# Kernel optimization log

Measured on AMD Instinct MI355X. Metric: run time of the kernel, lower is better.

The kernel has to match this reference:

```python
import jax, jax.numpy as jnp
import numpy as np

HIDDEN = 2048
HEADS = 16
HEAD_DIM = HIDDEN // HEADS
BATCH = 2
SEQ = 2048
ROPE_BASE = 10000.0


def _rope_cos_sin(seq_len, head_dim, dtype):
    inv_freq = 1.0 / (ROPE_BASE ** (jnp.arange(0, head_dim, 2, dtype=jnp.float32) / head_dim))
    t = jnp.arange(seq_len, dtype=jnp.float32)
    freqs = jnp.outer(t, inv_freq)                 # [S, D/2]
    emb = jnp.concatenate([freqs, freqs], axis=-1)  # [S, D]
    return jnp.cos(emb).astype(dtype), jnp.sin(emb).astype(dtype)


def _rotate_half(x):
    x1, x2 = jnp.split(x, 2, axis=-1)
    return jnp.concatenate([-x2, x1], axis=-1)


def setup_inputs() -> dict:
    key = jax.random.key(0)
    ks = jax.random.split(key, 5)
    scale = 1.0 / np.sqrt(HIDDEN)
    return {
        "x": jax.random.normal(ks[0], (BATCH, SEQ, HIDDEN), dtype=jnp.float32),
        "Wq": jax.random.normal(ks[1], (HIDDEN, HIDDEN), dtype=jnp.float32) * scale,
        "Wk": jax.random.normal(ks[2], (HIDDEN, HIDDEN), dtype=jnp.float32) * scale,
        "Wv": jax.random.normal(ks[3], (HIDDEN, HIDDEN), dtype=jnp.float32) * scale,
        "Wo": jax.random.normal(ks[4], (HIDDEN, HIDDEN), dtype=jnp.float32) * scale,
    }


def reference(x, Wq, Wk, Wv, Wo):
    B, S, H = x.shape
    # projections (torch Linear: y = x @ W.T)
    q = jnp.einsum('bsh,oh->bso', x, Wq).reshape(B, S, HEADS, HEAD_DIM).transpose(0, 2, 1, 3)
    k = jnp.einsum('bsh,oh->bso', x, Wk).reshape(B, S, HEADS, HEAD_DIM).transpose(0, 2, 1, 3)
    v = jnp.einsum('bsh,oh->bso', x, Wv).reshape(B, S, HEADS, HEAD_DIM).transpose(0, 2, 1, 3)
    # RoPE
    cos, sin = _rope_cos_sin(S, HEAD_DIM, x.dtype)  # [S, D]
    cos = cos[None, None]  # [1,1,S,D]
    sin = sin[None, None]
    q = q * cos + _rotate_half(q) * sin
    k = k * cos + _rotate_half(k) * sin
    # attention scores [B, H, S, S]
    scale = HEAD_DIM ** -0.5
    scores = jnp.einsum('bhqd,bhkd->bhqk', q, k) * scale
    causal = jnp.triu(jnp.ones((S, S), dtype=bool), k=1)  # kv_len==seq -> diagonal=1
    scores = jnp.where(causal[None, None], -jnp.inf, scores)
    attn = jax.nn.softmax(scores.astype(jnp.float32), axis=-1).astype(q.dtype)
    # dropout is identity in eval mode
    out = jnp.einsum('bhqk,bhkd->bhqd', attn, v)  # [B,H,S,D]
    out = out.transpose(0, 2, 1, 3).reshape(B, S, H)
    return jnp.einsum('bsh,oh->bso', out, Wo)
```

## Files before the change

kernel.cpp:

```cpp
#include <hip/hip_runtime.h>
#include <hip/hip_bf16.h>
#include <cstdint>
#include <cstddef>

constexpr int HIDDEN = 2048;
constexpr int HEADS  = 16;
constexpr int HD     = 128;
constexpr int BATCH  = 2;
constexpr int SEQ    = 2048;
constexpr int MROWS  = BATCH * SEQ;

typedef __attribute__((ext_vector_type(8))) short bf16x8;
typedef __attribute__((ext_vector_type(4))) float f32x4;

__device__ __forceinline__ unsigned short f2bf(float f) {
  union { float f; unsigned int u; } c; c.f = f;
  unsigned int r = c.u + 0x7FFFu + ((c.u >> 16) & 1u);
  return (unsigned short)(r >> 16);
}
__device__ __forceinline__ unsigned short f2bft(float f) {
  union { float f; unsigned int u; } c; c.f = f;
  return (unsigned short)(c.u >> 16);
}
__device__ __forceinline__ float bf2f(unsigned short u) {
  union { unsigned int u; float f; } c; c.u = ((unsigned int)u) << 16;
  return c.f;
}

__device__ __forceinline__ void gload_lds16(const void* g, void* l) {
  __builtin_amdgcn_global_load_lds(
      (const __attribute__((address_space(1))) void*)g,
      (__attribute__((address_space(3))) void*)l, 16, 0, 0);
}

__global__ void k_cvt(const float* __restrict__ in, unsigned short* __restrict__ out, int n4) {
  int i = blockIdx.x * 256 + threadIdx.x;
  if (i >= n4) return;
  float4 v = reinterpret_cast<const float4*>(in)[i];
  ushort4 o;
  o.x = f2bf(v.x); o.y = f2bf(v.y); o.z = f2bf(v.z); o.w = f2bf(v.w);
  reinterpret_cast<ushort4*>(out)[i] = o;
}

__global__ void k_cvtw(const float* __restrict__ w0, const float* __restrict__ w1,
                       const float* __restrict__ w2, const float* __restrict__ w3,
                       unsigned short* __restrict__ out) {
  constexpr int N4W = HIDDEN * HIDDEN / 4;
  int idx = blockIdx.x * 256 + threadIdx.x;
  int seg = idx >> 20;
  int off = idx & (N4W - 1);
  const float* src = (seg == 0) ? w0 : (seg == 1) ? w1 : (seg == 2) ? w2 : w3;
  float4 v = reinterpret_cast<const float4*>(src)[off];
  ushort4 o;
  o.x = f2bf(v.x); o.y = f2bf(v.y); o.z = f2bf(v.z); o.w = f2bf(v.w);
  reinterpret_cast<ushort4*>(out)[idx] = o;
}

template<int MODE>
__global__ __launch_bounds__(256, 2) void k_gemm(const unsigned short* __restrict__ A,
                                                 const unsigned short* __restrict__ Bm,
                                                 void* __restrict__ Cout,
                                                 int M, int N, int K) {
  __shared__ unsigned short As[128 * 32];
  __shared__ unsigned short Bs[128 * 32];
  const int t    = threadIdx.x;
  const int lane = t & 63;
  const int w    = t >> 6;
  const int wr   = w >> 1, wc = w & 1;
  const int m0   = blockIdx.y * 128;
  const int n0   = blockIdx.x * 128;
  const int l15  = lane & 15, lg = lane >> 4;

  f32x4 acc[4][4];
#pragma unroll
  for (int mi = 0; mi < 4; ++mi)
#pragma unroll
    for (int ni = 0; ni < 4; ++ni)
#pragma unroll
      for (int r = 0; r < 4; ++r) acc[mi][ni][r] = 0.f;

  const int rowA = t >> 2;
  const int col8 = (t & 3) * 8;
  const unsigned short* gA0 = A  + (size_t)(m0 + rowA) * K + col8;
  const unsigned short* gA1 = gA0 + (size_t)64 * K;
  const unsigned short* gB0 = Bm + (size_t)(n0 + rowA) * K + col8;
  const unsigned short* gB1 = gB0 + (size_t)64 * K;
  unsigned short* lA0 = As + t * 8;
  unsigned short* lA1 = As + 64 * 32 + t * 8;
  unsigned short* lB0 = Bs + t * 8;
  unsigned short* lB1 = Bs + 64 * 32 + t * 8;

  for (int k0 = 0; k0 < K; k0 += 32) {
    gload_lds16(gA0 + k0, lA0);
    gload_lds16(gA1 + k0, lA1);
    gload_lds16(gB0 + k0, lB0);
    gload_lds16(gB1 + k0, lB1);
    __syncthreads();

    bf16x8 a[4], b[4];
#pragma unroll
    for (int i = 0; i < 4; ++i)
      a[i] = *reinterpret_cast<const bf16x8*>(&As[(wr * 64 + i * 16 + l15) * 32 + lg * 8]);
#pragma unroll
    for (int i = 0; i < 4; ++i)
      b[i] = *reinterpret_cast<const bf16x8*>(&Bs[(wc * 64 + i * 16 + l15) * 32 + lg * 8]);
#pragma unroll
    for (int mi = 0; mi < 4; ++mi)
#pragma unroll
      for (int ni = 0; ni < 4; ++ni)
        acc[mi][ni] = __builtin_amdgcn_mfma_f32_16x16x32_bf16(a[mi], b[ni], acc[mi][ni], 0, 0, 0);
    __syncthreads();
  }

#pragma unroll
  for (int mi = 0; mi < 4; ++mi) {
#pragma unroll
    for (int ni = 0; ni < 4; ++ni) {
#pragma unroll
      for (int r = 0; r < 4; ++r) {
        int row = m0 + wr * 64 + mi * 16 + lg * 4 + r;
        int col = n0 + wc * 64 + ni * 16 + l15;
        float v = acc[mi][ni][r];
        if (MODE == 2) {
          reinterpret_cast<float*>(Cout)[(size_t)row * N + col] = v;
        } else if (MODE == 0) {
          int b = row >> 11, s = row & (SEQ - 1);
          int which = col >> 11;
          int hc = col & 2047;
          int h = hc >> 7, d = hc & (HD - 1);
          size_t addr = (size_t)which * ((size_t)MROWS * HIDDEN)
                      + ((size_t)(b * HEADS + h) * SEQ + s) * HD + d;
          reinterpret_cast<unsigned short*>(Cout)[addr] = f2bf(v);
        } else {
          int h = row >> 7, d = row & (HD - 1);
          int b = col >> 11, s = col & (SEQ - 1);
          size_t addr = ((size_t)(b * HEADS + h) * HD + d) * SEQ + s;
          reinterpret_cast<unsigned short*>(Cout)[addr] = f2bf(v);
        }
      }
    }
  }
}

constexpr float QSCALE = 0.08838834764831845f * 1.4426950408889634f;

__global__ void k_rope(unsigned short* __restrict__ Qb, unsigned short* __restrict__ Kb) {
  int idx = blockIdx.x * 256 + threadIdx.x;
  int c  = idx & 7;
  int s  = (idx >> 3) & (SEQ - 1);
  int bh = idx >> 14;
  size_t base = ((size_t)bh * SEQ + s) * HD + c * 8;

  bf16x8 ql = *reinterpret_cast<const bf16x8*>(Qb + base);
  bf16x8 qh = *reinterpret_cast<const bf16x8*>(Qb + base + 64);
  bf16x8 kl = *reinterpret_cast<const bf16x8*>(Kb + base);
  bf16x8 kh = *reinterpret_cast<const bf16x8*>(Kb + base + 64);
  bf16x8 qlo, qho, klo, kho;
#pragma unroll
  for (int j = 0; j < 8; ++j) {
    float d   = (float)(c * 8 + j);
    float ang = (float)s * expf(d * -0.14391156511756683f);
    float sn, cs;
    __sincosf(ang, &sn, &cs);
    float a0 = bf2f((unsigned short)ql[j]), a1 = bf2f((unsigned short)qh[j]);
    qlo[j] = (short)f2bf((a0 * cs - a1 * sn) * QSCALE);
    qho[j] = (short)f2bf((a1 * cs + a0 * sn) * QSCALE);
    float b0 = bf2f((unsigned short)kl[j]), b1 = bf2f((unsigned short)kh[j]);
    klo[j] = (short)f2bf(b0 * cs - b1 * sn);
    kho[j] = (short)f2bf(b1 * cs + b0 * sn);
  }
  *reinterpret_cast<bf16x8*>(Qb + base)      = qlo;
  *reinterpret_cast<bf16x8*>(Qb + base + 64) = qho;
  *reinterpret_cast<bf16x8*>(Kb + base)      = klo;
  *reinterpret_cast<bf16x8*>(Kb + base + 64) = kho;
}

constexpr int QB  = 128;
constexpr int KVB = 64;
constexpr int NQT = SEQ / QB;

__global__ __launch_bounds__(512)
__attribute__((amdgpu_waves_per_eu(4, 4)))
void k_attn(const unsigned short* __restrict__ Q,
            const unsigned short* __restrict__ Kk,
            const unsigned short* __restrict__ Vt,
            unsigned short* __restrict__ O) {
  __shared__ char lds[2 * 16384 + 2 * 16384 + 16384];
  char* Ks = lds;
  char* Vs = lds + 2 * 16384;
  char* Ps = lds + 4 * 16384;

  const int t    = threadIdx.x;
  const int lane = t & 63;
  const int w    = t >> 6;
  const int l15  = lane & 15, lg = lane >> 4;
  const int bh   = blockIdx.y;
  const int b    = bh >> 4, h = bh & 15;
  const int qt   = (bh >= HEADS) ? (NQT - 1 - (int)blockIdx.x) : (int)blockIdx.x;
  const int q0b  = qt * QB;
  const int q0w  = q0b + w * 16;
  const int qw_hi = q0w + 15;

  const unsigned short* Qb = Q  + (size_t)bh * SEQ * HD;
  const unsigned short* Kb = Kk + (size_t)bh * SEQ * HD;
  const unsigned short* Vb = Vt + (size_t)bh * HD * SEQ;

  bf16x8 qf[4];
#pragma unroll
  for (int c = 0; c < 4; ++c)
    qf[c] = *reinterpret_cast<const bf16x8*>(Qb + (size_t)(q0w + l15) * HD + c * 32 + lg * 8);

  float mrow[4], lpart[4];
  f32x4 oacc[8];
#pragma unroll
  for (int r = 0; r < 4; ++r) { mrow[r] = -1e30f; lpart[r] = 0.f; }
#pragma unroll
  for (int dt = 0; dt < 8; ++dt)
#pragma unroll
    for (int r = 0; r < 4; ++r) oacc[dt][r] = 0.f;

  const int sp     = t * 16;
  const int srow   = sp >> 8;
  const int scolb  = (sp & 255) ^ ((srow & 7) << 4);
  const unsigned short* ksrc2 = Kb + (size_t)srow * HD + (scolb >> 1);
  char* kdst2 = Ks + sp;

  const int vrow  = t >> 3;
  const int vcolb = ((t & 7) << 4) ^ ((vrow & 7) << 4);
  const unsigned short* vsrc = Vb + (size_t)vrow * SEQ + (vcolb >> 1);
  char* vdst = Vs + t * 16;

  const int nb = q0b / KVB + 2;

  gload_lds16(ksrc2, kdst2);
  gload_lds16(ksrc2 + (size_t)32 * HD, kdst2 + 8192);
  gload_lds16(vsrc, vdst);
  gload_lds16(vsrc + (size_t)64 * SEQ, vdst + 8192);
  __syncthreads();

  int cur = 0;
  for (int kb = 0; kb < nb; ++kb) {
    const int kv0 = kb * KVB;
    if (kb + 1 < nb) {
      const int nxt = kv0 + KVB;
      char* nk = kdst2 + (cur ^ 1) * 16384;
      char* nv = vdst  + (cur ^ 1) * 16384;
      gload_lds16(ksrc2 + (size_t)nxt * HD, nk);
      gload_lds16(ksrc2 + (size_t)(nxt + 32) * HD, nk + 8192);
      gload_lds16(vsrc + nxt, nv);
      gload_lds16(vsrc + (size_t)64 * SEQ + nxt, nv + 8192);
    }

    if (kv0 <= qw_hi) {
      const char* Kc = Ks + cur * 16384;
      const char* Vc = Vs + cur * 16384;
      f32x4 sc[4];
#pragma unroll
      for (int tt = 0; tt < 4; ++tt)
#pragma unroll
        for (int r = 0; r < 4; ++r) sc[tt][r] = 0.f;
      __builtin_amdgcn_s_setprio(1);
#pragma unroll
      for (int tt = 0; tt < 4; ++tt) {
        const int kr = tt * 16 + l15;
        const int xr = (kr & 7) << 4;
#pragma unroll
        for (int c = 0; c < 4; ++c) {
          bf16x8 kf = *reinterpret_cast<const bf16x8*>(
              Kc + kr * 256 + ((c * 64 + lg * 16) ^ xr));
          sc[tt] = __builtin_amdgcn_mfma_f32_16x16x32_bf16(qf[c], kf, sc[tt], 0, 0, 0);
        }
      }
      __builtin_amdgcn_s_setprio(0);

      const bool full = (kv0 + KVB - 1 <= q0w);
#pragma unroll
      for (int r = 0; r < 4; ++r) {
        const int qg = q0w + lg * 4 + r;
        float v0 = sc[0][r], v1 = sc[1][r];
        float v2 = sc[2][r], v3 = sc[3][r];
        if (!full) {
          if (kv0 +      l15 > qg) v0 = -1e30f;
          if (kv0 + 16 + l15 > qg) v1 = -1e30f;
          if (kv0 + 32 + l15 > qg) v2 = -1e30f;
          if (kv0 + 48 + l15 > qg) v3 = -1e30f;
        }
        float pm = fmaxf(fmaxf(v0, v1), fmaxf(v2, v3));
        if (__any(pm > mrow[r] + 11.5f)) {
          float pmr = pm;
          pmr = fmaxf(pmr, __shfl_xor(pmr, 1));
          pmr = fmaxf(pmr, __shfl_xor(pmr, 2));
          pmr = fmaxf(pmr, __shfl_xor(pmr, 4));
          pmr = fmaxf(pmr, __shfl_xor(pmr, 8));
          float mn = fmaxf(mrow[r], pmr);
          float al = exp2f(mrow[r] - mn);
          lpart[r] *= al;
#pragma unroll
          for (int dt = 0; dt < 8; ++dt) oacc[dt][r] *= al;
          mrow[r] = mn;
        }
        float p0 = exp2f(v0 - mrow[r]);
        float p1 = exp2f(v1 - mrow[r]);
        float p2 = exp2f(v2 - mrow[r]);
        float p3 = exp2f(v3 - mrow[r]);
        lpart[r] += (p0 + p1) + (p2 + p3);
        const int prow = lg * 4 + r;
        const int xpr  = (prow & 7) << 4;
        char* pw = Ps + w * 2048 + prow * 128;
        *reinterpret_cast<unsigned short*>(pw + (((0 * 32) + l15 * 2) ^ xpr)) = f2bft(p0);
        *reinterpret_cast<unsigned short*>(pw + (((1 * 32) + l15 * 2) ^ xpr)) = f2bft(p1);
        *reinterpret_cast<unsigned short*>(pw + (((2 * 32) + l15 * 2) ^ xpr)) = f2bft(p2);
        *reinterpret_cast<unsigned short*>(pw + (((3 * 32) + l15 * 2) ^ xpr)) = f2bft(p3);
      }
      asm volatile("s_waitcnt lgkmcnt(0)" ::: "memory");

      const int xq = (l15 & 7) << 4;
      const char* pr = Ps + w * 2048 + l15 * 128;
      bf16x8 pa0 = *reinterpret_cast<const bf16x8*>(pr + ((0  + lg * 16) ^ xq));
      bf16x8 pa1 = *reinterpret_cast<const bf16x8*>(pr + ((64 + lg * 16) ^ xq));
      const int xv = (l15 & 7) << 4;
      __builtin_amdgcn_s_setprio(1);
#pragma unroll
      for (int dt = 0; dt < 8; ++dt) {
        const char* vrl = Vc + (dt * 16 + l15) * 128;
        bf16x8 vf0 = *reinterpret_cast<const bf16x8*>(vrl + ((lg * 16) ^ xv));
        bf16x8 vf1 = *reinterpret_cast<const bf16x8*>(vrl + ((64 + lg * 16) ^ xv));
        oacc[dt] = __builtin_amdgcn_mfma_f32_16x16x32_bf16(pa0, vf0, oacc[dt], 0, 0, 0);
        oacc[dt] = __builtin_amdgcn_mfma_f32_16x16x32_bf16(pa1, vf1, oacc[dt], 0, 0, 0);
      }
      __builtin_amdgcn_s_setprio(0);
    }
    __syncthreads();
    cur ^= 1;
  }

  float inv[4];
#pragma unroll
  for (int r = 0; r < 4; ++r) {
    float ls = lpart[r];
    ls += __shfl_xor(ls, 1);
    ls += __shfl_xor(ls, 2);
    ls += __shfl_xor(ls, 4);
    ls += __shfl_xor(ls, 8);
    inv[r] = 1.0f / ls;
  }
#pragma unroll
  for (int dt = 0; dt < 8; ++dt) {
#pragma unroll
    for (int r = 0; r < 4; ++r) {
      int qg = q0w + lg * 4 + r;
      int dv = dt * 16 + l15;
      O[((size_t)(b * SEQ + qg) * HEADS + h) * HD + dv] = f2bf(oacc[dt][r] * inv[r]);
    }
  }
}

extern "C" void kernel_launch(void* const* d_in, const int* in_sizes, int n_in,
                              void* d_out, int out_size, void* d_ws, size_t ws_size,
                              hipStream_t stream) {
  (void)in_sizes; (void)n_in; (void)out_size; (void)ws_size;
  const float* x  = (const float*)d_in[0];
  const float* Wq = (const float*)d_in[1];
  const float* Wk = (const float*)d_in[2];
  const float* Wv = (const float*)d_in[3];
  const float* Wo = (const float*)d_in[4];
  float* out = (float*)d_out;

  unsigned short* xb  = (unsigned short*)d_ws;
  unsigned short* wqb = xb  + (size_t)MROWS * HIDDEN;
  unsigned short* wkb = wqb + (size_t)HIDDEN * HIDDEN;
  unsigned short* wvb = wkb + (size_t)HIDDEN * HIDDEN;
  unsigned short* wob = wvb + (size_t)HIDDEN * HIDDEN;
  unsigned short* Qb  = wob + (size_t)HIDDEN * HIDDEN;
  unsigned short* Kb  = Qb  + (size_t)MROWS * HIDDEN;
  unsigned short* Vtb = Kb  + (size_t)MROWS * HIDDEN;
  unsigned short* Ob  = Vtb + (size_t)MROWS * HIDDEN;

  int n4x = MROWS * HIDDEN / 4;
  k_cvt<<<(n4x + 255) / 256, 256, 0, stream>>>(x, xb, n4x);
  k_cvtw<<<(4 * HIDDEN * HIDDEN / 4) / 256, 256, 0, stream>>>(Wq, Wk, Wv, Wo, wqb);

  dim3 gQK(4096 / 128, MROWS / 128);
  k_gemm<0><<<gQK, 256, 0, stream>>>(xb, wqb, Qb, MROWS, 4096, HIDDEN);
  dim3 gV(MROWS / 128, HIDDEN / 128);
  k_gemm<3><<<gV, 256, 0, stream>>>(wvb, xb, Vtb, HIDDEN, MROWS, HIDDEN);

  k_rope<<<(BATCH * HEADS * SEQ * 8) / 256, 256, 0, stream>>>(Qb, Kb);

  k_attn<<<dim3(SEQ / QB, BATCH * HEADS), 512, 0, stream>>>(Qb, Kb, Vtb, Ob);

  dim3 gO(HIDDEN / 128, MROWS / 128);
  k_gemm<2><<<gO, 256, 0, stream>>>(Ob, wob, out, MROWS, HIDDEN, HIDDEN);
}
```

Baseline: 279.2 us.

## Add 256x256 double-buffered QK projection GEMM and merge conversion kernels

Replaces the 128x128-tile GEMM for the fused Q/K projection with a dedicated 512-thread kernel. It uses 256x256 tiles, direct global-to-LDS loads with an XOR swizzle, a two-stage LDS double buffer, s_setprio around the MFMA blocks, and a remapped block order for L2 locality. The x and weight fp32-to-bf16 conversions are merged into one launch. The goal is more operand reuse per loaded byte, overlap of loads with MFMA work, and one fewer kernel launch. The cost is 128 KB of LDS per block and heavy register pressure, which limits occupancy.

After: 258.6 us. -7.4%, faster.

```diff
diff --git a/kernel.cpp b/kernel.cpp
--- a/kernel.cpp
+++ b/kernel.cpp
@@ -33,27 +33,162 @@
       (__attribute__((address_space(3))) void*)l, 16, 0, 0);
 }
 
-__global__ void k_cvt(const float* __restrict__ in, unsigned short* __restrict__ out, int n4) {
-  int i = blockIdx.x * 256 + threadIdx.x;
-  if (i >= n4) return;
-  float4 v = reinterpret_cast<const float4*>(in)[i];
-  ushort4 o;
-  o.x = f2bf(v.x); o.y = f2bf(v.y); o.z = f2bf(v.z); o.w = f2bf(v.w);
-  reinterpret_cast<ushort4*>(out)[i] = o;
-}
-
-__global__ void k_cvtw(const float* __restrict__ w0, const float* __restrict__ w1,
-                       const float* __restrict__ w2, const float* __restrict__ w3,
-                       unsigned short* __restrict__ out) {
+__global__ void k_cvt_all(const float* __restrict__ x,
+                          const float* __restrict__ w0, const float* __restrict__ w1,
+                          const float* __restrict__ w2, const float* __restrict__ w3,
+                          unsigned short* __restrict__ out) {
+  constexpr int N4X = MROWS * HIDDEN / 4;
   constexpr int N4W = HIDDEN * HIDDEN / 4;
   int idx = blockIdx.x * 256 + threadIdx.x;
-  int seg = idx >> 20;
-  int off = idx & (N4W - 1);
-  const float* src = (seg == 0) ? w0 : (seg == 1) ? w1 : (seg == 2) ? w2 : w3;
+  const float* src;
+  int off;
+  if (idx < N4X) { src = x; off = idx; }
+  else {
+    int j = idx - N4X;
+    int seg = j >> 20;
+    off = j & (N4W - 1);
+    src = (seg == 0) ? w0 : (seg == 1) ? w1 : (seg == 2) ? w2 : w3;
+  }
   float4 v = reinterpret_cast<const float4*>(src)[off];
   ushort4 o;
   o.x = f2bf(v.x); o.y = f2bf(v.y); o.z = f2bf(v.z); o.w = f2bf(v.w);
   reinterpret_cast<ushort4*>(out)[idx] = o;
+}
+
+constexpr int GK  = 2048;
+constexpr int GNT = GK / 64;
+
+__global__ __launch_bounds__(512)
+__attribute__((amdgpu_waves_per_eu(2)))
+void k_gemm256(const unsigned short* __restrict__ A,
+               const unsigned short* __restrict__ Bm,
+               unsigned short* __restrict__ Cout) {
+  __shared__ char lds[131072];
+  char* ldsA = lds;
+  char* ldsB = lds + 65536;
+
+  const int t    = threadIdx.x;
+  const int lane = t & 63;
+  const int w    = t >> 6;
+  const int wr   = w >> 2;
+  const int wc   = w & 3;
+  const int l15  = lane & 15, lg = lane >> 4;
+
+  const int orig = blockIdx.x;
+  const int wg   = (orig & 7) * 32 + (orig >> 3);
+  const int m0   = (wg >> 4) * 256;
+  const int n0   = (wg & 15) * 256;
+
+  const int rowA = t >> 3;
+  const int xsel = ((t & 7) ^ (rowA & 7)) * 8;
+  const unsigned short* aS = A  + (size_t)(m0 + rowA) * GK + xsel;
+  const unsigned short* bS = Bm + (size_t)(n0 + rowA) * GK + xsel;
+  char* aD = ldsA + t * 16;
+  char* bD = ldsB + t * 16;
+
+#define STAGE256(buf, kt) do {                                   \
+    const unsigned short* ap = aS + (kt) * 64;                   \
+    const unsigned short* bp = bS + (kt) * 64;                   \
+    char* ad = aD + (buf) * 32768;                               \
+    char* bd = bD + (buf) * 32768;                               \
+    gload_lds16(ap,                  ad);                        \
+    gload_lds16(ap + 64 * GK,        ad + 8192);                 \
+    gload_lds16(ap + 128 * GK,       ad + 16384);                \
+    gload_lds16(ap + 192 * GK,       ad + 24576);                \
+    gload_lds16(bp,                  bd);                        \
+    gload_lds16(bp + 64 * GK,        bd + 8192);                 \
+    gload_lds16(bp + 128 * GK,       bd + 16384);                \
+    gload_lds16(bp + 192 * GK,       bd + 24576);                \
+  } while (0)
+
+  const int xr  = (l15 & 7) << 4;
+  const int vo0 = (lg * 16) ^ xr;
+  const int vo1 = (64 + lg * 16) ^ xr;
+  const char* aR = ldsA + wr * 16384 + l15 * 128;
+  const char* bR = ldsB + (wc >> 1) * 16384 + (wc & 1) * 8192 + l15 * 128;
+
+  f32x4 acc[8][4];
+#pragma unroll
+  for (int mi = 0; mi < 8; ++mi)
+#pragma unroll
+    for (int ni = 0; ni < 4; ++ni)
+#pragma unroll
+      for (int r = 0; r < 4; ++r) acc[mi][ni][r] = 0.f;
+
+  STAGE256(0, 0);
+  STAGE256(1, 1);
+  asm volatile("s_waitcnt vmcnt(8)" ::: "memory");
+  __builtin_amdgcn_s_barrier();
+  asm volatile("" ::: "memory");
+
+#pragma unroll 1
+  for (int kt = 0; kt < GNT; ++kt) {
+    const int buf = kt & 1;
+    const char* a = aR + buf * 32768;
+    const char* b = bR + buf * 32768;
+
+    bf16x8 af0[8], bf0[4];
+#pragma unroll
+    for (int mi = 0; mi < 8; ++mi)
+      af0[mi] = *reinterpret_cast<const bf16x8*>(a + mi * 2048 + vo0);
+#pragma unroll
+    for (int ni = 0; ni < 4; ++ni)
+      bf0[ni] = *reinterpret_cast<const bf16x8*>(b + ni * 2048 + vo0);
+    __builtin_amdgcn_s_setprio(1);
+#pragma unroll
+    for (int mi = 0; mi < 8; ++mi)
+#pragma unroll
+      for (int ni = 0; ni < 4; ++ni)
+        acc[mi][ni] = __builtin_amdgcn_mfma_f32_16x16x32_bf16(af0[mi], bf0[ni], acc[mi][ni], 0, 0, 0);
+    __builtin_amdgcn_s_setprio(0);
+
+    bf16x8 af1[8], bf1[4];
+#pragma unroll
+    for (int mi = 0; mi < 8; ++mi)
+      af1[mi] = *reinterpret_cast<const bf16x8*>(a + mi * 2048 + vo1);
+#pragma unroll
+    for (int ni = 0; ni < 4; ++ni)
+      bf1[ni] = *reinterpret_cast<const bf16x8*>(b + ni * 2048 + vo1);
+
+    asm volatile("s_waitcnt lgkmcnt(0)" ::: "memory");
+    __builtin_amdgcn_s_barrier();
+    asm volatile("" ::: "memory");
+
+    if (kt < GNT - 2) STAGE256(buf, kt + 2);
+
+    __builtin_amdgcn_s_setprio(1);
+#pragma unroll
+    for (int mi = 0; mi < 8; ++mi)
+#pragma unroll
+      for (int ni = 0; ni < 4; ++ni)
+        acc[mi][ni] = __builtin_amdgcn_mfma_f32_16x16x32_bf16(af1[mi], bf1[ni], acc[mi][ni], 0, 0, 0);
+    __builtin_amdgcn_s_setprio(0);
+
+    if (kt < GNT - 2) asm volatile("s_waitcnt vmcnt(8)" ::: "memory");
+    else              asm volatile("s_waitcnt vmcnt(0)" ::: "memory");
+    __builtin_amdgcn_s_barrier();
+    asm volatile("" ::: "memory");
+  }
+#undef STAGE256
+
+#pragma unroll
+  for (int mi = 0; mi < 8; ++mi) {
+#pragma unroll
+    for (int ni = 0; ni < 4; ++ni) {
+#pragma unroll
+      for (int r = 0; r < 4; ++r) {
+        int row = m0 + wr * 128 + mi * 16 + lg * 4 + r;
+        int col = n0 + wc * 64 + ni * 16 + l15;
+        int bb = row >> 11, s = row & (SEQ - 1);
+        int which = col >> 11;
+        int hc = col & 2047;
+        int h = hc >> 7, d = hc & (HD - 1);
+        size_t addr = (size_t)which * ((size_t)MROWS * HIDDEN)
+                    + ((size_t)(bb * HEADS + h) * SEQ + s) * HD + d;
+        Cout[addr] = f2bf(acc[mi][ni][r]);
+      }
+    }
+  }
 }
 
 template<int MODE>
@@ -123,14 +258,6 @@
         float v = acc[mi][ni][r];
         if (MODE == 2) {
           reinterpret_cast<float*>(Cout)[(size_t)row * N + col] = v;
-        } else if (MODE == 0) {
-          int b = row >> 11, s = row & (SEQ - 1);
-          int which = col >> 11;
-          int hc = col & 2047;
-          int h = hc >> 7, d = hc & (HD - 1);
-          size_t addr = (size_t)which * ((size_t)MROWS * HIDDEN)
-                      + ((size_t)(b * HEADS + h) * SEQ + s) * HD + d;
-          reinterpret_cast<unsigned short*>(Cout)[addr] = f2bf(v);
         } else {
           int h = row >> 7, d = row & (HD - 1);
           int b = col >> 11, s = col & (SEQ - 1);
@@ -376,12 +503,10 @@
   unsigned short* Vtb = Kb  + (size_t)MROWS * HIDDEN;
   unsigned short* Ob  = Vtb + (size_t)MROWS * HIDDEN;
 
-  int n4x = MROWS * HIDDEN / 4;
-  k_cvt<<<(n4x + 255) / 256, 256, 0, stream>>>(x, xb, n4x);
-  k_cvtw<<<(4 * HIDDEN * HIDDEN / 4) / 256, 256, 0, stream>>>(Wq, Wk, Wv, Wo, wqb);
-
-  dim3 gQK(4096 / 128, MROWS / 128);
-  k_gemm<0><<<gQK, 256, 0, stream>>>(xb, wqb, Qb, MROWS, 4096, HIDDEN);
+  constexpr int CVT_THREADS = (MROWS * HIDDEN + 4 * HIDDEN * HIDDEN) / 4;
+  k_cvt_all<<<CVT_THREADS / 256, 256, 0, stream>>>(x, Wq, Wk, Wv, Wo, xb);
+
+  k_gemm256<<<256, 512, 0, stream>>>(xb, wqb, Qb);
   dim3 gV(MROWS / 128, HIDDEN / 128);
   k_gemm<3><<<gV, 256, 0, stream>>>(wvb, xb, Vtb, HIDDEN, MROWS, HIDDEN);
 
```
